# Kernel optimization log

Measured on AMD Instinct MI355X. Metric: run time of the kernel, lower is better.

Reference implementation:

```python
import jax, jax.numpy as jnp
import numpy as np

H = 16      # num_heads
D = 64      # nhid (per-head dim)
SL, BS = 1024, 64
DM = 1024   # keys_dim == query_dim == values_dim

def setup_inputs() -> dict:
    key = jax.random.key(0)
    k1, k2, k3, k4, k5 = jax.random.split(key, 5)
    return {
        "query":  jax.random.normal(k1, (BS, DM), dtype=jnp.float32),
        "keys":   jax.random.normal(k2, (SL, BS, DM), dtype=jnp.float32),
        "values": jax.random.normal(k3, (SL, BS, DM), dtype=jnp.float32),
        "Wq":     jax.random.normal(k4, (H * D, DM), dtype=jnp.float32) * 0.02,
        "Wk":     jax.random.normal(k5, (H * D, DM), dtype=jnp.float32) * 0.02,
    }

def reference(query, keys, values, Wq, Wk):
    bs = query.shape[0]
    sl = keys.shape[0]
    scale = jnp.asarray(np.sqrt(D), dtype=query.dtype)
    # projections (note: original module applies keys_linear to values -- a bug we replicate)
    qp = (query @ Wq.T).reshape(bs, H, D)                 # [bs, H, D]
    kp = (keys @ Wk.T).reshape(sl, bs, H, D)              # [sl, bs, H, D]
    vp = (values @ Wk.T).reshape(sl, bs, H, D)            # [sl, bs, H, D]
    # per-head scaled dot-product scores, softmax over the sequence axis (dim 0)
    scores = jnp.einsum('bhd,sbhd->sbh', qp, kp) / scale  # [sl, bs, H]
    attn = jax.nn.softmax(scores, axis=0)
    out = jnp.einsum('sbh,sbhd->bhd', attn, vp)           # [bs, H, D]
    return out.reshape(bs, H * D)
```

## Files before the change

### kernel.cpp

```cpp
#include <hip/hip_runtime.h>
#include <cstddef>
#include <cstdint>

#define NH 16
#define HD 64
#define SLEN 1024
#define NB 64
#define DMODEL 1024

#define DOT4_ACC(acc, k, q) \
  acc = fmaf((k).x, (q).x, fmaf((k).y, (q).y, fmaf((k).z, (q).z, fmaf((k).w, (q).w, (acc)))))

#define FMA4_BCAST(accv, qv, w0_, w1_, w2_, w3_) do { \
  (accv).x = fmaf((qv).x, (w0_).x, fmaf((qv).y, (w1_).x, fmaf((qv).z, (w2_).x, fmaf((qv).w, (w3_).x, (accv).x)))); \
  (accv).y = fmaf((qv).x, (w0_).y, fmaf((qv).y, (w1_).y, fmaf((qv).z, (w2_).y, fmaf((qv).w, (w3_).y, (accv).y)))); \
  (accv).z = fmaf((qv).x, (w0_).z, fmaf((qv).y, (w1_).z, fmaf((qv).z, (w2_).z, fmaf((qv).w, (w3_).z, (accv).z)))); \
  (accv).w = fmaf((qv).x, (w0_).w, fmaf((qv).y, (w1_).w, fmaf((qv).z, (w2_).w, fmaf((qv).w, (w3_).w, (accv).w)))); \
} while (0)

#define VMCNT_WAIT(n) asm volatile("s_waitcnt vmcnt(" #n ")" ::: "memory")
#define BAR() asm volatile("s_barrier" ::: "memory")

__device__ __forceinline__ float wred_sum(float v) {
#pragma unroll
  for (int off = 32; off; off >>= 1) v += __shfl_xor(v, off, 64);
  return v;
}

__device__ __forceinline__ void gload16(const float* g, float* lds_base) {
  __builtin_amdgcn_global_load_lds(
      (const __attribute__((address_space(1))) void*)g,
      (__attribute__((address_space(3))) void*)lds_base, 16, 0, 0);
}

__global__ __launch_bounds__(256) void k0_qp(const float* __restrict__ query,
                                             const float* __restrict__ Wq,
                                             float* __restrict__ qp) {
  const int tid = threadIdx.x;
  const int w = tid >> 6, l = tid & 63;
  const int jq = blockIdx.x & 255;
  const int bq = blockIdx.x >> 8;
  const int j = jq * 4 + w;
  const float4* wr = reinterpret_cast<const float4*>(Wq + (size_t)j * DMODEL) + l * 4;
  const float4 w0 = wr[0], w1 = wr[1], w2 = wr[2], w3 = wr[3];
  float acc[16];
#pragma unroll
  for (int bi = 0; bi < 16; ++bi) {
    const float4* qr = reinterpret_cast<const float4*>(
        query + (size_t)(bq * 16 + bi) * DMODEL) + l * 4;
    float4 q0 = qr[0], q1 = qr[1], q2 = qr[2], q3 = qr[3];
    float s = 0.f;
    DOT4_ACC(s, w0, q0); DOT4_ACC(s, w1, q1); DOT4_ACC(s, w2, q2); DOT4_ACC(s, w3, q3);
    acc[bi] = s;
  }
#pragma unroll
  for (int off = 32; off; off >>= 1) {
#pragma unroll
    for (int bi = 0; bi < 16; ++bi) acc[bi] += __shfl_xor(acc[bi], off, 64);
  }
  if (l == 0) {
#pragma unroll
    for (int bi = 0; bi < 16; ++bi)
      qp[(size_t)(bq * 16 + bi) * DMODEL + j] = acc[bi];
  }
}

__global__ __launch_bounds__(256) void k1_qt(const float* __restrict__ qp,
                                             const float* __restrict__ Wk,
                                             float* __restrict__ qt) {
  __shared__ __align__(16) float qpl[2][HD];
  const int h = blockIdx.x & 15;
  const int b0 = (blockIdx.x >> 4) * 2;
  const int tid = threadIdx.x;
  if (tid < 2 * HD) qpl[tid >> 6][tid & 63] =
      qp[(size_t)(b0 + (tid >> 6)) * DMODEL + h * HD + (tid & 63)];
  __syncthreads();
  const int m4 = tid * 4;
  float4 acc0 = make_float4(0.f, 0.f, 0.f, 0.f);
  float4 acc1 = make_float4(0.f, 0.f, 0.f, 0.f);
  const float* wbase = Wk + (size_t)(h * HD) * DMODEL + m4;
  for (int d = 0; d < HD; d += 4) {
    float4 wk0 = *reinterpret_cast<const float4*>(wbase + (size_t)(d + 0) * DMODEL);
    float4 wk1 = *reinterpret_cast<const float4*>(wbase + (size_t)(d + 1) * DMODEL);
    float4 wk2 = *reinterpret_cast<const float4*>(wbase + (size_t)(d + 2) * DMODEL);
    float4 wk3 = *reinterpret_cast<const float4*>(wbase + (size_t)(d + 3) * DMODEL);
    float4 qa = *reinterpret_cast<const float4*>(&qpl[0][d]);
    float4 qb = *reinterpret_cast<const float4*>(&qpl[1][d]);
    FMA4_BCAST(acc0, qa, wk0, wk1, wk2, wk3);
    FMA4_BCAST(acc1, qb, wk0, wk1, wk2, wk3);
  }
  *reinterpret_cast<float4*>(qt + ((size_t)(b0 + 0) * NH + h) * DMODEL + m4) = acc0;
  *reinterpret_cast<float4*>(qt + ((size_t)(b0 + 1) * NH + h) * DMODEL + m4) = acc1;
}

__global__ __launch_bounds__(256) void k2_scores(const float* __restrict__ keys,
                                                 const float* __restrict__ qt,
                                                 float* __restrict__ scp) {
  __shared__ __align__(16) float kb[2][64 * 64];
  __shared__ __align__(16) float qb[2][NH * 64];
  const int b  = blockIdx.x & 63;
  const int st = (blockIdx.x >> 6) & 15;
  const int mh = blockIdx.x >> 10;
  const int tid = threadIdx.x, w = tid >> 6, l = tid & 63;
  const int hg = l & 3;
  const int rg = (l >> 2) & 3;
  const int hq = l >> 4;
  const int s0 = st * 64;
  const size_t rowstride = (size_t)NB * DMODEL;
  const float* kbase = keys + ((size_t)s0 * NB + b) * DMODEL + mh * 512;
  const float* qbase = qt + (size_t)b * NH * DMODEL + mh * 512;
  const int srow4 = l >> 4;
  const int sslot = l & 15;

#define K2_STAGE(buf_, ch_) do {                                               \
    _Pragma("unroll")                                                          \
    for (int i_ = 0; i_ < 4; ++i_) {                                           \
      const int r_ = w * 16 + i_ * 4 + srow4;                                  \
      gload16(kbase + (size_t)r_ * rowstride + (ch_) * 64 +                    \
                  ((sslot ^ (r_ & 7)) << 2),                                   \
              &kb[buf_][(w * 16 + i_ * 4) * 64]);                              \
    }                                                                          \
    gload16(qbase + (size_t)(w * 4 + srow4) * DMODEL + (ch_) * 64 +            \
                ((sslot ^ (w << 2)) << 2),                                     \
            &qb[buf_][w * 4 * 64]);                                            \
  } while (0)

  float acc[4][4];
#pragma unroll
  for (int r = 0; r < 4; ++r)
#pragma unroll
    for (int h = 0; h < 4; ++h) acc[r][h] = 0.f;

  K2_STAGE(0, 0);
  for (int ch = 0; ch < 8; ++ch) {
    const int buf = ch & 1;
    if (ch + 1 < 8) {
      K2_STAGE(buf ^ 1, ch + 1);
      VMCNT_WAIT(5);
    } else {
      VMCNT_WAIT(0);
    }
    BAR();
#pragma unroll
    for (int j = 0; j < 4; ++j) {
      float4 kv[4], qv[4];
#pragma unroll
      for (int r = 0; r < 4; ++r) {
        const int row = w * 16 + rg * 4 + r;
        kv[r] = *reinterpret_cast<const float4*>(
            &kb[buf][row * 64 + (((hg + 4 * j) ^ (row & 7)) << 2)]);
      }
#pragma unroll
      for (int h = 0; h < 4; ++h) {
        const int hh = hq * 4 + h;
        qv[h] = *reinterpret_cast<const float4*>(
            &qb[buf][hh * 64 + (((hg + 4 * j) ^ (hq << 2)) << 2)]);
      }
#pragma unroll
      for (int r = 0; r < 4; ++r)
#pragma unroll
        for (int h = 0; h < 4; ++h)
          DOT4_ACC(acc[r][h], kv[r], qv[h]);
    }
    BAR();
  }
#undef K2_STAGE
#pragma unroll
  for (int r = 0; r < 4; ++r)
#pragma unroll
    for (int h = 0; h < 4; ++h) {
      acc[r][h] += __shfl_xor(acc[r][h], 1, 64);
      acc[r][h] += __shfl_xor(acc[r][h], 2, 64);
    }
  const float scale = 0.125f;
  float* plane = scp + (size_t)mh * NB * NH * SLEN;
  float* orow = plane + ((size_t)b * NH + hq * 4 + hg) * SLEN + s0 + w * 16 + rg * 4;
#pragma unroll
  for (int r = 0; r < 4; ++r) {
    float v = hg == 0 ? acc[r][0] : hg == 1 ? acc[r][1]
            : hg == 2 ? acc[r][2] : acc[r][3];
    orow[r] = v * scale;
  }
}

__global__ __launch_bounds__(256) void k_sm(float* __restrict__ sc0,
                                            const float* __restrict__ sc1) {
  __shared__ float red[8];
  const int tid = threadIdx.x, w = tid >> 6, l = tid & 63;
  float* p0 = sc0 + (size_t)blockIdx.x * SLEN;
  const float* p1 = sc1 + (size_t)blockIdx.x * SLEN;
  float4 xa = reinterpret_cast<const float4*>(p0)[tid];
  float4 xb = reinterpret_cast<const float4*>(p1)[tid];
  float4 x = make_float4(xa.x + xb.x, xa.y + xb.y, xa.z + xb.z, xa.w + xb.w);
  float mx = fmaxf(fmaxf(x.x, x.y), fmaxf(x.z, x.w));
#pragma unroll
  for (int off = 32; off; off >>= 1) mx = fmaxf(mx, __shfl_xor(mx, off, 64));
  if (l == 0) red[w] = mx;
  __syncthreads();
  mx = fmaxf(fmaxf(red[0], red[1]), fmaxf(red[2], red[3]));
  float4 e;
  e.x = __expf(x.x - mx); e.y = __expf(x.y - mx);
  e.z = __expf(x.z - mx); e.w = __expf(x.w - mx);
  float sum = e.x + e.y + e.z + e.w;
  sum = wred_sum(sum);
  if (l == 0) red[4 + w] = sum;
  __syncthreads();
  sum = red[4] + red[5] + red[6] + red[7];
  const float inv = 1.f / sum;
  e.x *= inv; e.y *= inv; e.z *= inv; e.w *= inv;
  reinterpret_cast<float4*>(p0)[tid] = e;
}

template <int NCH>
__global__ __launch_bounds__(256) void k3_cpart(const float* __restrict__ values,
                                                const float* __restrict__ attn,
                                                float* __restrict__ cp) {
  constexpr int SC = SLEN / NCH;
  __shared__ __align__(16) float vb[2][4][DMODEL];
  __shared__ __align__(16) float al[NH][SC];
  const int b = blockIdx.x & 63;
  const int ch = blockIdx.x >> 6;
  const int s0 = ch * SC;
  const int tid = threadIdx.x, w = tid >> 6, l = tid & 63;
  for (int f = tid; f < NH * (SC / 4); f += 256) {
    int hh = f / (SC / 4), c4 = (f % (SC / 4)) * 4;
    *reinterpret_cast<float4*>(&al[hh][c4]) = *reinterpret_cast<const float4*>(
        attn + ((size_t)b * NH + hh) * SLEN + s0 + c4);
  }
  const int m4 = tid * 4;
  float4 acc[NH];
#pragma unroll
  for (int i = 0; i < NH; ++i) acc[i] = make_float4(0.f, 0.f, 0.f, 0.f);
  const size_t rowstride = (size_t)NB * DMODEL;
  const float* vbase = values + ((size_t)s0 * NB + b) * DMODEL;

#define K3_STAGE(buf_, g_) do {                                               \
    const float* rg_ = vbase + (size_t)((g_) * 4 + w) * rowstride;            \
    _Pragma("unroll")                                                         \
    for (int j_ = 0; j_ < 4; ++j_)                                            \
      gload16(rg_ + j_ * 256 + l * 4, &vb[buf_][w][j_ * 256]);                \
  } while (0)

  K3_STAGE(0, 0);
  __syncthreads();
  for (int g = 0; g < SC / 4; ++g) {
    const int buf = g & 1;
    if (g + 1 < SC / 4) {
      K3_STAGE(buf ^ 1, g + 1);
      VMCNT_WAIT(4);
    } else {
      VMCNT_WAIT(0);
    }
    BAR();
    float4 v0 = *reinterpret_cast<const float4*>(&vb[buf][0][m4]);
    float4 v1 = *reinterpret_cast<const float4*>(&vb[buf][1][m4]);
    float4 v2 = *reinterpret_cast<const float4*>(&vb[buf][2][m4]);
    float4 v3 = *reinterpret_cast<const float4*>(&vb[buf][3][m4]);
#pragma unroll
    for (int hh = 0; hh < NH; ++hh) {
      float4 av = *reinterpret_cast<const float4*>(&al[hh][g * 4]);
      FMA4_BCAST(acc[hh], av, v0, v1, v2, v3);
    }
    BAR();
  }
#undef K3_STAGE
#pragma unroll
  for (int hh = 0; hh < NH; ++hh)
    *reinterpret_cast<float4*>(cp + (((size_t)ch * NB + b) * NH + hh) * DMODEL + m4) = acc[hh];
}

template <int NCH>
__global__ __launch_bounds__(256) void k4_out(const float* __restrict__ cp,
                                              const float* __restrict__ Wk,
                                              float* __restrict__ out) {
  __shared__ __align__(16) float cl[2 * DMODEL];
  const int h = blockIdx.x & 15;
  const int b0 = (blockIdx.x >> 4) * 2;
  const int tid = threadIdx.x, w = tid >> 6, l = tid & 63;
  for (int f = tid; f < 2 * DMODEL / 4; f += 256) {
    int bi = f >> 8, m4 = (f & 255) * 4;
    float4 s = make_float4(0.f, 0.f, 0.f, 0.f);
#pragma unroll
    for (int ch = 0; ch < NCH; ++ch) {
      float4 t = *reinterpret_cast<const float4*>(
          cp + (((size_t)ch * NB + b0 + bi) * NH + h) * DMODEL + m4);
      s.x += t.x; s.y += t.y; s.z += t.z; s.w += t.w;
    }
    *reinterpret_cast<float4*>(&cl[bi * DMODEL + m4]) = s;
  }
  __syncthreads();
  float4 c[2][4];
#pragma unroll
  for (int bi = 0; bi < 2; ++bi)
#pragma unroll
    for (int k = 0; k < 4; ++k)
      c[bi][k] = *reinterpret_cast<const float4*>(&cl[bi * DMODEL + l * 16 + k * 4]);
  for (int jj = 0; jj < 16; ++jj) {
    const int d = w * 16 + jj;
    const float4* wr = reinterpret_cast<const float4*>(Wk + (size_t)(h * HD + d) * DMODEL) + l * 4;
    const float4 w0 = wr[0], w1 = wr[1], w2 = wr[2], w3 = wr[3];
#pragma unroll
    for (int bi = 0; bi < 2; ++bi) {
      float s = 0.f;
      DOT4_ACC(s, w0, c[bi][0]); DOT4_ACC(s, w1, c[bi][1]);
      DOT4_ACC(s, w2, c[bi][2]); DOT4_ACC(s, w3, c[bi][3]);
      s = wred_sum(s);
      if (l == 0) out[(size_t)(b0 + bi) * (NH * HD) + h * HD + d] = s;
    }
  }
}

extern "C" void kernel_launch(void* const* d_in, const int* in_sizes, int n_in,
                              void* d_out, int out_size, void* d_ws, size_t ws_size,
                              hipStream_t stream) {
  const float* query  = (const float*)d_in[0];
  const float* keys   = (const float*)d_in[1];
  const float* values = (const float*)d_in[2];
  const float* Wq     = (const float*)d_in[3];
  const float* Wk     = (const float*)d_in[4];
  float* out = (float*)d_out;

  float* W   = (float*)d_ws;
  float* qp  = W;
  float* qt  = qp + (size_t)NB * DMODEL;
  float* sc0 = qt + (size_t)NB * NH * DMODEL;
  float* sc1 = sc0 + (size_t)NB * NH * SLEN;
  float* cp  = sc1 + (size_t)NB * NH * SLEN;

  const size_t base_floats = (size_t)NB * DMODEL + (size_t)NB * NH * DMODEL
                           + 2 * (size_t)NB * NH * SLEN;

  k0_qp<<<1024, 256, 0, stream>>>(query, Wq, qp);
  k1_qt<<<512, 256, 0, stream>>>(qp, Wk, qt);
  k2_scores<<<2048, 256, 0, stream>>>(keys, qt, sc0);
  k_sm<<<NB * NH, 256, 0, stream>>>(sc0, sc1);

  const size_t chunk_floats = (size_t)NB * NH * DMODEL;
  if (ws_size >= (base_floats + 16 * chunk_floats) * sizeof(float)) {
    k3_cpart<16><<<16 * NB, 256, 0, stream>>>(values, sc0, cp);
    k4_out<16><<<NH * (NB / 2), 256, 0, stream>>>(cp, Wk, out);
  } else if (ws_size >= (base_floats + 8 * chunk_floats) * sizeof(float)) {
    k3_cpart<8><<<8 * NB, 256, 0, stream>>>(values, sc0, cp);
    k4_out<8><<<NH * (NB / 2), 256, 0, stream>>>(cp, Wk, out);
  } else {
    k3_cpart<4><<<4 * NB, 256, 0, stream>>>(values, sc0, cp);
    k4_out<4><<<NH * (NB / 2), 256, 0, stream>>>(cp, Wk, out);
  }
}
```

Measured before the change: 208.9 us.

## Enlarge k2_scores register tile to 8x8 with 256-row sequence blocks

Restructures the scores kernel so each block covers 256 sequence rows instead of 64, with 32-wide feature chunks. Each thread now computes an 8-row by 8-head accumulator tile, up from 4x4, raising arithmetic per LDS load and cutting the grid from 2048 to 512 blocks. The swizzle and wait counts are reworked to match. The kernel is memory-bound on streaming keys, so the gain may be small, and the larger register tile and fewer blocks could lower occupancy and latency hiding.

```diff
diff --git a/kernel.cpp b/kernel.cpp
--- a/kernel.cpp
+++ b/kernel.cpp
@@ -93,93 +93,98 @@
   *reinterpret_cast<float4*>(qt + ((size_t)(b0 + 1) * NH + h) * DMODEL + m4) = acc1;
 }
 
-__global__ __launch_bounds__(256) void k2_scores(const float* __restrict__ keys,
-                                                 const float* __restrict__ qt,
-                                                 float* __restrict__ scp) {
-  __shared__ __align__(16) float kb[2][64 * 64];
-  __shared__ __align__(16) float qb[2][NH * 64];
+__global__ __launch_bounds__(256, 2) void k2_scores(const float* __restrict__ keys,
+                                                    const float* __restrict__ qt,
+                                                    float* __restrict__ scp) {
+  __shared__ __align__(16) float kb[2][256 * 32];
+  __shared__ __align__(16) float qb[2][NH * 32];
   const int b  = blockIdx.x & 63;
-  const int st = (blockIdx.x >> 6) & 15;
-  const int mh = blockIdx.x >> 10;
+  const int st = (blockIdx.x >> 6) & 3;
+  const int mh = blockIdx.x >> 8;
   const int tid = threadIdx.x, w = tid >> 6, l = tid & 63;
-  const int hg = l & 3;
-  const int rg = (l >> 2) & 3;
-  const int hq = l >> 4;
-  const int s0 = st * 64;
+  const int ms = l & 3;
+  const int rg = (l >> 2) & 7;
+  const int hq = l >> 5;
+  const int s0 = st * 256;
   const size_t rowstride = (size_t)NB * DMODEL;
   const float* kbase = keys + ((size_t)s0 * NB + b) * DMODEL + mh * 512;
   const float* qbase = qt + (size_t)b * NH * DMODEL + mh * 512;
-  const int srow4 = l >> 4;
-  const int sslot = l & 15;
+  const int srow  = l >> 3;
+  const int sslot = l & 7;
 
 #define K2_STAGE(buf_, ch_) do {                                               \
     _Pragma("unroll")                                                          \
-    for (int i_ = 0; i_ < 4; ++i_) {                                           \
-      const int r_ = w * 16 + i_ * 4 + srow4;                                  \
-      gload16(kbase + (size_t)r_ * rowstride + (ch_) * 64 +                    \
-                  ((sslot ^ (r_ & 7)) << 2),                                   \
-              &kb[buf_][(w * 16 + i_ * 4) * 64]);                              \
+    for (int i_ = 0; i_ < 8; ++i_) {                                           \
+      const int r_ = w * 64 + i_ * 8 + srow;                                   \
+      gload16(kbase + (size_t)r_ * rowstride + (ch_) * 32 +                    \
+                  ((sslot ^ srow) << 2),                                       \
+              &kb[buf_][(w * 64 + i_ * 8) * 32]);                              \
     }                                                                          \
-    gload16(qbase + (size_t)(w * 4 + srow4) * DMODEL + (ch_) * 64 +            \
-                ((sslot ^ (w << 2)) << 2),                                     \
-            &qb[buf_][w * 4 * 64]);                                            \
+    if (w < 2)                                                                 \
+      gload16(qbase + (size_t)(w * 8 + srow) * DMODEL + (ch_) * 32 +           \
+                  ((sslot ^ srow) << 2),                                       \
+              &qb[buf_][w * 8 * 32]);                                          \
   } while (0)
 
-  float acc[4][4];
-#pragma unroll
-  for (int r = 0; r < 4; ++r)
-#pragma unroll
-    for (int h = 0; h < 4; ++h) acc[r][h] = 0.f;
+  float acc[8][8];
+#pragma unroll
+  for (int r = 0; r < 8; ++r)
+#pragma unroll
+    for (int h = 0; h < 8; ++h) acc[r][h] = 0.f;
 
   K2_STAGE(0, 0);
-  for (int ch = 0; ch < 8; ++ch) {
+  for (int ch = 0; ch < 16; ++ch) {
     const int buf = ch & 1;
-    if (ch + 1 < 8) {
+    if (ch + 1 < 16) {
       K2_STAGE(buf ^ 1, ch + 1);
-      VMCNT_WAIT(5);
+      if (w < 2) { VMCNT_WAIT(9); } else { VMCNT_WAIT(8); }
     } else {
       VMCNT_WAIT(0);
     }
     BAR();
 #pragma unroll
-    for (int j = 0; j < 4; ++j) {
-      float4 kv[4], qv[4];
-#pragma unroll
-      for (int r = 0; r < 4; ++r) {
-        const int row = w * 16 + rg * 4 + r;
+    for (int j = 0; j < 2; ++j) {
+      const int c = j * 4 + ms;
+      float4 kv[8], qv[8];
+#pragma unroll
+      for (int r = 0; r < 8; ++r) {
+        const int row = w * 64 + rg * 8 + r;
         kv[r] = *reinterpret_cast<const float4*>(
-            &kb[buf][row * 64 + (((hg + 4 * j) ^ (row & 7)) << 2)]);
+            &kb[buf][row * 32 + ((c ^ r) << 2)]);
       }
 #pragma unroll
-      for (int h = 0; h < 4; ++h) {
-        const int hh = hq * 4 + h;
+      for (int h = 0; h < 8; ++h) {
+        const int hh = hq * 8 + h;
         qv[h] = *reinterpret_cast<const float4*>(
-            &qb[buf][hh * 64 + (((hg + 4 * j) ^ (hq << 2)) << 2)]);
+            &qb[buf][hh * 32 + ((c ^ h) << 2)]);
       }
 #pragma unroll
-      for (int r = 0; r < 4; ++r)
-#pragma unroll
-        for (int h = 0; h < 4; ++h)
+      for (int r = 0; r < 8; ++r)
+#pragma unroll
+        for (int h = 0; h < 8; ++h)
           DOT4_ACC(acc[r][h], kv[r], qv[h]);
     }
     BAR();
   }
 #undef K2_STAGE
 #pragma unroll
-  for (int r = 0; r < 4; ++r)
-#pragma unroll
-    for (int h = 0; h < 4; ++h) {
+  for (int r = 0; r < 8; ++r)
+#pragma unroll
+    for (int h = 0; h < 8; ++h) {
       acc[r][h] += __shfl_xor(acc[r][h], 1, 64);
       acc[r][h] += __shfl_xor(acc[r][h], 2, 64);
     }
   const float scale = 0.125f;
   float* plane = scp + (size_t)mh * NB * NH * SLEN;
-  float* orow = plane + ((size_t)b * NH + hq * 4 + hg) * SLEN + s0 + w * 16 + rg * 4;
-#pragma unroll
-  for (int r = 0; r < 4; ++r) {
-    float v = hg == 0 ? acc[r][0] : hg == 1 ? acc[r][1]
-            : hg == 2 ? acc[r][2] : acc[r][3];
-    orow[r] = v * scale;
+#pragma unroll
+  for (int r = 0; r < 8; ++r) {
+#pragma unroll
+    for (int t = 0; t < 2; ++t) {
+      float v = ms == 0 ? acc[r][t] : ms == 1 ? acc[r][2 + t]
+              : ms == 2 ? acc[r][4 + t] : acc[r][6 + t];
+      plane[((size_t)b * NH + hq * 8 + ms * 2 + t) * SLEN
+            + s0 + w * 64 + rg * 8 + r] = v * scale;
+    }
   }
 }
 
@@ -332,7 +337,7 @@
 
   k0_qp<<<1024, 256, 0, stream>>>(query, Wq, qp);
   k1_qt<<<512, 256, 0, stream>>>(qp, Wk, qt);
-  k2_scores<<<2048, 256, 0, stream>>>(keys, qt, sc0);
+  k2_scores<<<512, 256, 0, stream>>>(keys, qt, sc0);
   k_sm<<<NB * NH, 256, 0, stream>>>(sc0, sc1);
 
   const size_t chunk_floats = (size_t)NB * NH * DMODEL;
```

Result: no change. 207.4 us (-0.7%).

## Restructure score kernel to stage full-width key rows with resident query tile

Applied to the files above, without the earlier changes.

The scores kernel now loads all 16 heads' 512-wide query slice into shared memory once. It then streams keys in groups of 8 rows at full 512-dim width with double buffering, so each warp owns two rows and needs no block barrier inside the loop. Partial dot products are reduced across 16 lanes by shuffles and written out per group, replacing the earlier 64-dim chunk loop with a single reduction at the end. This cuts barriers and adds a two-blocks-per-CU launch bound, at the cost of more shuffle work, scattered scalar stores and more shared memory per block.

```diff
diff --git a/kernel.cpp b/kernel.cpp
--- a/kernel.cpp
+++ b/kernel.cpp
@@ -93,94 +93,96 @@
   *reinterpret_cast<float4*>(qt + ((size_t)(b0 + 1) * NH + h) * DMODEL + m4) = acc1;
 }
 
-__global__ __launch_bounds__(256) void k2_scores(const float* __restrict__ keys,
-                                                 const float* __restrict__ qt,
-                                                 float* __restrict__ scp) {
-  __shared__ __align__(16) float kb[2][64 * 64];
-  __shared__ __align__(16) float qb[2][NH * 64];
+__global__ __launch_bounds__(256, 2) void k2_scores(const float* __restrict__ keys,
+                                                    const float* __restrict__ qt,
+                                                    float* __restrict__ scp) {
+  __shared__ __align__(16) float qb[NH][512];
+  __shared__ __align__(16) float kb[2][8][512];
   const int b  = blockIdx.x & 63;
   const int st = (blockIdx.x >> 6) & 15;
   const int mh = blockIdx.x >> 10;
   const int tid = threadIdx.x, w = tid >> 6, l = tid & 63;
-  const int hg = l & 3;
-  const int rg = (l >> 2) & 3;
-  const int hq = l >> 4;
+  const int mg = l & 15;
+  const int hg = l >> 4;
   const int s0 = st * 64;
   const size_t rowstride = (size_t)NB * DMODEL;
   const float* kbase = keys + ((size_t)s0 * NB + b) * DMODEL + mh * 512;
   const float* qbase = qt + (size_t)b * NH * DMODEL + mh * 512;
-  const int srow4 = l >> 4;
-  const int sslot = l & 15;
-
-#define K2_STAGE(buf_, ch_) do {                                               \
+
+#pragma unroll
+  for (int i = 0; i < 4; ++i) {
+    const int hh = w * 4 + i;
+    const float* qrow = qbase + (size_t)hh * DMODEL;
+#pragma unroll
+    for (int c = 0; c < 2; ++c)
+      gload16(qrow + (size_t)(c * 64 + (l ^ hh)) * 4, &qb[hh][c * 256]);
+  }
+
+#define K2_STAGE(buf_, g_) do {                                                \
     _Pragma("unroll")                                                          \
-    for (int i_ = 0; i_ < 4; ++i_) {                                           \
-      const int r_ = w * 16 + i_ * 4 + srow4;                                  \
-      gload16(kbase + (size_t)r_ * rowstride + (ch_) * 64 +                    \
-                  ((sslot ^ (r_ & 7)) << 2),                                   \
-              &kb[buf_][(w * 16 + i_ * 4) * 64]);                              \
+    for (int i_ = 0; i_ < 2; ++i_) {                                           \
+      const int sr_ = (g_) * 8 + w * 2 + i_;                                   \
+      const float* kr_ = kbase + (size_t)sr_ * rowstride;                      \
+      _Pragma("unroll")                                                        \
+      for (int c_ = 0; c_ < 2; ++c_)                                           \
+        gload16(kr_ + (size_t)(c_ * 64 + l) * 4,                               \
+                &kb[buf_][w * 2 + i_][c_ * 256]);                              \
     }                                                                          \
-    gload16(qbase + (size_t)(w * 4 + srow4) * DMODEL + (ch_) * 64 +            \
-                ((sslot ^ (w << 2)) << 2),                                     \
-            &qb[buf_][w * 4 * 64]);                                            \
   } while (0)
 
-  float acc[4][4];
-#pragma unroll
-  for (int r = 0; r < 4; ++r)
-#pragma unroll
-    for (int h = 0; h < 4; ++h) acc[r][h] = 0.f;
-
   K2_STAGE(0, 0);
-  for (int ch = 0; ch < 8; ++ch) {
-    const int buf = ch & 1;
-    if (ch + 1 < 8) {
-      K2_STAGE(buf ^ 1, ch + 1);
-      VMCNT_WAIT(5);
+  VMCNT_WAIT(0);
+  __syncthreads();
+
+  const float scale = 0.125f;
+  float* plane = scp + (size_t)mh * NB * NH * SLEN;
+
+  for (int g = 0; g < 8; ++g) {
+    const int buf = g & 1;
+    if (g + 1 < 8) {
+      K2_STAGE(buf ^ 1, g + 1);
+      VMCNT_WAIT(4);
     } else {
       VMCNT_WAIT(0);
     }
-    BAR();
-#pragma unroll
-    for (int j = 0; j < 4; ++j) {
-      float4 kv[4], qv[4];
-#pragma unroll
-      for (int r = 0; r < 4; ++r) {
-        const int row = w * 16 + rg * 4 + r;
-        kv[r] = *reinterpret_cast<const float4*>(
-            &kb[buf][row * 64 + (((hg + 4 * j) ^ (row & 7)) << 2)]);
+    float acc[2][4];
+#pragma unroll
+    for (int r = 0; r < 2; ++r)
+#pragma unroll
+      for (int h = 0; h < 4; ++h) acc[r][h] = 0.f;
+#pragma unroll
+    for (int p = 0; p < 8; ++p) {
+      float4 kv0 = *reinterpret_cast<const float4*>(
+          &kb[buf][w * 2 + 0][(p * 16 + mg) * 4]);
+      float4 kv1 = *reinterpret_cast<const float4*>(
+          &kb[buf][w * 2 + 1][(p * 16 + mg) * 4]);
+      float4 qv[4];
+#pragma unroll
+      for (int h = 0; h < 4; ++h) {
+        const int hh = hg * 4 + h;
+        qv[h] = *reinterpret_cast<const float4*>(
+            &qb[hh][(p * 16 + (mg ^ hh)) * 4]);
       }
 #pragma unroll
       for (int h = 0; h < 4; ++h) {
-        const int hh = hq * 4 + h;
-        qv[h] = *reinterpret_cast<const float4*>(
-            &qb[buf][hh * 64 + (((hg + 4 * j) ^ (hq << 2)) << 2)]);
+        DOT4_ACC(acc[0][h], kv0, qv[h]);
+        DOT4_ACC(acc[1][h], kv1, qv[h]);
       }
-#pragma unroll
-      for (int r = 0; r < 4; ++r)
+    }
+#pragma unroll
+    for (int off = 1; off <= 8; off <<= 1)
+#pragma unroll
+      for (int r = 0; r < 2; ++r)
 #pragma unroll
         for (int h = 0; h < 4; ++h)
-          DOT4_ACC(acc[r][h], kv[r], qv[h]);
-    }
-    BAR();
+          acc[r][h] += __shfl_xor(acc[r][h], off, 64);
+    if (mg < 8) {
+      const int r = mg >> 2, h = mg & 3;
+      plane[((size_t)b * NH + hg * 4 + h) * SLEN + s0 + g * 8 + w * 2 + r] =
+          acc[r][h] * scale;
+    }
   }
 #undef K2_STAGE
-#pragma unroll
-  for (int r = 0; r < 4; ++r)
-#pragma unroll
-    for (int h = 0; h < 4; ++h) {
-      acc[r][h] += __shfl_xor(acc[r][h], 1, 64);
-      acc[r][h] += __shfl_xor(acc[r][h], 2, 64);
-    }
-  const float scale = 0.125f;
-  float* plane = scp + (size_t)mh * NB * NH * SLEN;
-  float* orow = plane + ((size_t)b * NH + hq * 4 + hg) * SLEN + s0 + w * 16 + rg * 4;
-#pragma unroll
-  for (int r = 0; r < 4; ++r) {
-    float v = hg == 0 ? acc[r][0] : hg == 1 ? acc[r][1]
-            : hg == 2 ? acc[r][2] : acc[r][3];
-    orow[r] = v * scale;
-  }
 }
 
 __global__ __launch_bounds__(256) void k_sm(float* __restrict__ sc0,
```

New measurement: 233.5 us. 11.8% more time.
